# Kernel optimization log

Measured on AMD Instinct MI355X. Metric: run time of the kernel, lower is better.

## Reference

```python
import jax, jax.numpy as jnp
import numpy as np

N_NODES = 50000  # nodes in the (sub)graph


def setup_inputs() -> dict:
    key = jax.random.key(0)
    ks = jax.random.split(key, 8)
    nodes = jax.random.randint(ks[0], (N_NODES,), 0, 100000)
    src = jax.random.randint(ks[1], (800000,), 0, N_NODES)
    dst = jax.random.randint(ks[2], (800000,), 0, N_NODES)
    emb = jax.random.normal(ks[3], (100000, 256), dtype=jnp.float32)
    W = jax.random.normal(ks[4], (256, 128), dtype=jnp.float32) * 0.05
    b = jax.random.normal(ks[5], (128,), dtype=jnp.float32) * 0.05
    mlp_w = jax.random.normal(ks[6], (128, 40), dtype=jnp.float32) * 0.05
    mlp_b = jax.random.normal(ks[7], (40,), dtype=jnp.float32) * 0.05
    return {"nodes": nodes, "src": src, "dst": dst, "emb": emb,
            "W": W, "b": b, "mlp_w": mlp_w, "mlp_b": mlp_b}


def reference(nodes, src, dst, emb, W, b, mlp_w, mlp_b):
    n = N_NODES
    ones = jnp.ones_like(src, dtype=jnp.float32)
    out_deg = jax.ops.segment_sum(ones, src, num_segments=n)  # src out-degree
    in_deg = jax.ops.segment_sum(ones, dst, num_segments=n)   # dst in-degree
    norm_src = jax.lax.rsqrt(jnp.maximum(out_deg, 1.0))       # D_out^{-1/2}
    norm_dst = jax.lax.rsqrt(jnp.maximum(in_deg, 1.0))        # D_in^{-1/2}

    feat = emb[nodes]                                          # [N, in_dim]
    # dgl GraphConv(norm='both'): in_dim > out_dim -> project first, then aggregate
    h = (feat * norm_src[:, None]) @ W                         # [N, out_dim]
    agg = jax.ops.segment_sum(h[src], dst, num_segments=n)     # SpMM: sum over in-edges
    feat_out = agg * norm_dst[:, None] + b                     # [N, out_dim]

    logits = feat_out @ mlp_w + mlp_b                          # [N, num_classes]
    return (feat_out, logits)
```

## Files before the change

### kernel.cpp

```cpp
#include <hip/hip_runtime.h>

#define IN_DIM 256
#define OUT_DIM 128
#define N_CLS 40

#define SLICE 16384
#define NE_CH 40

typedef __attribute__((ext_vector_type(8))) short short8;
typedef __attribute__((ext_vector_type(4))) float floatx4;

static __device__ __forceinline__ unsigned short f2bf(float f) {
    union { float f; unsigned u; } v; v.f = f;
    unsigned r = v.u + 0x7FFF + ((v.u >> 16) & 1);
    return (unsigned short)(r >> 16);
}

static __device__ __forceinline__ unsigned cvtpk(float lo, float hi) {
    unsigned r;
    asm("v_cvt_pk_bf16_f32 %0, %1, %2" : "=v"(r) : "v"(lo), "v"(hi));
    return r;
}

__global__ __launch_bounds__(256) void hist_wconv_kernel(
    const int* __restrict__ src, const int* __restrict__ dst,
    int* __restrict__ partial_out, int* __restrict__ partial_in,
    const float* __restrict__ W, unsigned short* __restrict__ Wt,
    int* __restrict__ done, int ne, int n, int chunk, int nbh)
{
    __shared__ __align__(16) int lh_out[SLICE];
    __shared__ __align__(16) int lh_in[SLICE];

    const int tid = threadIdx.x;

    if (blockIdx.x >= nbh) {
        if (blockIdx.x == (unsigned)nbh && tid == 0) *done = 0;
        int t = (blockIdx.x - nbh) * 256 + tid;
        if (t < IN_DIM * OUT_DIM) {
            int k = t >> 7, c = t & 127;
            Wt[c * IN_DIM + k] = f2bf(W[t]);
        }
        return;
    }

    const int s = blockIdx.x / NE_CH;
    const int e = blockIdx.x % NE_CH;
    const int lo = s * SLICE;
    const int hi = min(lo + SLICE, n);

    for (int i = tid; i < SLICE; i += 256) { lh_out[i] = 0; lh_in[i] = 0; }
    __syncthreads();

    const int start = e * chunk;
    const int end = min(start + chunk, ne);
    const int cnt4 = (end - start) >> 2;
    const int4* s4 = (const int4*)(src + start);
    const int4* d4 = (const int4*)(dst + start);
    for (int k = tid; k < cnt4; k += 256) {
        int4 sv = s4[k];
        int4 dv = d4[k];
        unsigned q;
        q = (unsigned)(sv.x - lo); if (q < SLICE) atomicAdd(&lh_out[q], 1);
        q = (unsigned)(sv.y - lo); if (q < SLICE) atomicAdd(&lh_out[q], 1);
        q = (unsigned)(sv.z - lo); if (q < SLICE) atomicAdd(&lh_out[q], 1);
        q = (unsigned)(sv.w - lo); if (q < SLICE) atomicAdd(&lh_out[q], 1);
        q = (unsigned)(dv.x - lo); if (q < SLICE) atomicAdd(&lh_in[q], 1);
        q = (unsigned)(dv.y - lo); if (q < SLICE) atomicAdd(&lh_in[q], 1);
        q = (unsigned)(dv.z - lo); if (q < SLICE) atomicAdd(&lh_in[q], 1);
        q = (unsigned)(dv.w - lo); if (q < SLICE) atomicAdd(&lh_in[q], 1);
    }
    for (int t = start + (cnt4 << 2) + tid; t < end; t += 256) {
        unsigned q;
        q = (unsigned)(src[t] - lo); if (q < SLICE) atomicAdd(&lh_out[q], 1);
        q = (unsigned)(dst[t] - lo); if (q < SLICE) atomicAdd(&lh_in[q], 1);
    }
    __syncthreads();

    const int cnt = hi - lo;
    const int c4 = cnt >> 2;
    int4* po = (int4*)(partial_out + (size_t)e * n + lo);
    int4* pi = (int4*)(partial_in + (size_t)e * n + lo);
    for (int i = tid; i < c4; i += 256) {
        po[i] = ((const int4*)lh_out)[i];
        pi[i] = ((const int4*)lh_in)[i];
    }
    for (int i = (c4 << 2) + tid; i < cnt; i += 256) {
        partial_out[(size_t)e * n + lo + i] = lh_out[i];
        partial_in[(size_t)e * n + lo + i] = lh_in[i];
    }
}

__global__ __launch_bounds__(256) void reduce_scan_kernel(
    int* __restrict__ partial_out, int* __restrict__ partial_in,
    int* __restrict__ cnt_out, int* __restrict__ row_start,
    int* __restrict__ bsum, int* __restrict__ boffs,
    int* __restrict__ done, int n)
{
    __shared__ int wsum[4];
    __shared__ int is_last;
    const int tid = threadIdx.x;
    const int lane = tid & 63, wid = tid >> 6;
    const int base = blockIdx.x * 1024 + tid * 4;

    int4 run = make_int4(0, 0, 0, 0);

    if (base + 4 <= n) {
        int4 sum = make_int4(0, 0, 0, 0);
#pragma unroll
        for (int e = 0; e < NE_CH; e++) {
            int4 v = *(const int4*)(partial_out + (size_t)e * n + base);
            sum.x += v.x; sum.y += v.y; sum.z += v.z; sum.w += v.w;
        }
        *(int4*)(cnt_out + base) = sum;

#pragma unroll
        for (int e = 0; e < NE_CH; e++) {
            int* p = partial_in + (size_t)e * n + base;
            int4 v = *(const int4*)p;
            *(int4*)p = run;
            run.x += v.x; run.y += v.y; run.z += v.z; run.w += v.w;
        }
    } else if (base <= n) {
        int rr[4] = {0, 0, 0, 0};
#pragma unroll
        for (int j = 0; j < 4; j++) {
            int pos = base + j;
            if (pos < n) {
                int sum = 0, r = 0;
                for (int e = 0; e < NE_CH; e++) {
                    sum += partial_out[(size_t)e * n + pos];
                    int v = partial_in[(size_t)e * n + pos];
                    partial_in[(size_t)e * n + pos] = r;
                    r += v;
                }
                cnt_out[pos] = sum;
                rr[j] = r;
            }
        }
        run.x = rr[0]; run.y = rr[1]; run.z = rr[2]; run.w = rr[3];
    }

    const int s = run.x + run.y + run.z + run.w;
    const int e1 = run.x, e2 = run.x + run.y, e3 = run.x + run.y + run.z;

    int incl = s;
#pragma unroll
    for (int off = 1; off < 64; off <<= 1) {
        int q = __shfl_up(incl, (unsigned)off, 64);
        if (lane >= off) incl += q;
    }
    if (lane == 63) wsum[wid] = incl;
    __syncthreads();
    int woff = 0;
    for (int w = 0; w < wid; ++w) woff += wsum[w];
    const int texcl = woff + incl - s;

    if (base + 4 <= n) {
        int4 o = make_int4(texcl, texcl + e1, texcl + e2, texcl + e3);
        *(int4*)(row_start + base) = o;
    } else if (base <= n) {
        const int eo[4] = {0, e1, e2, e3};
#pragma unroll
        for (int j = 0; j < 4; j++) {
            int pos = base + j;
            if (pos <= n) row_start[pos] = texcl + eo[j];
        }
    }
    if (tid == 0) bsum[blockIdx.x] = wsum[0] + wsum[1] + wsum[2] + wsum[3];

    __threadfence();
    if (tid == 0) {
        int prev = atomicAdd(done, 1);
        is_last = (prev == (int)gridDim.x - 1) ? 1 : 0;
    }
    __syncthreads();
    if (is_last && tid < 64) {
        __threadfence();
        const int nb = (int)gridDim.x;
        int carry = 0;
        for (int c = 0; c < nb; c += 64) {
            int i = c + lane;
            int v = (i < nb) ? bsum[i] : 0;
            int inc2 = v;
#pragma unroll
            for (int off = 1; off < 64; off <<= 1) {
                int q = __shfl_up(inc2, (unsigned)off, 64);
                if (lane >= off) inc2 += q;
            }
            if (i < nb) boffs[i] = carry + inc2 - v;
            carry += __shfl(inc2, 63, 64);
        }
        if (lane == 0) boffs[nb] = carry;
    }
}

__global__ __launch_bounds__(256) void scatter_gemm_kernel(
    const int* __restrict__ src, const int* __restrict__ dst,
    const int* __restrict__ row_start, const int* __restrict__ boffs,
    const int* __restrict__ prefix_in, int* __restrict__ csr_src,
    const int* __restrict__ nodes, const float* __restrict__ emb,
    const unsigned short* __restrict__ Wt, const int* __restrict__ cnt_out,
    unsigned short* __restrict__ h,
    int ne, int n, int chunk, int nbh)
{
    __shared__ __align__(16) char smem[SLICE * 4];

    const int tid = threadIdx.x;

    if (blockIdx.x < (unsigned)nbh) {
        int* cur = (int*)smem;
        const int s = blockIdx.x / NE_CH;
        const int e = blockIdx.x % NE_CH;
        const int lo = s * SLICE;
        const int hi = min(lo + SLICE, n);
        const int cnt = hi - lo;

        const int c4 = cnt >> 2;
        for (int i = tid; i < c4; i += 256) {
            int idx4 = lo + i * 4;
            int4 rs = *(const int4*)(row_start + idx4);
            int4 pf = *(const int4*)(prefix_in + (size_t)e * n + idx4);
            const int bo = boffs[idx4 >> 10];
            rs.x += pf.x + bo; rs.y += pf.y + bo;
            rs.z += pf.z + bo; rs.w += pf.w + bo;
            ((int4*)cur)[i] = rs;
        }
        for (int i = (c4 << 2) + tid; i < cnt; i += 256) {
            int pos = lo + i;
            cur[i] = row_start[pos] + boffs[pos >> 10]
                   + prefix_in[(size_t)e * n + pos];
        }
        __syncthreads();

        const int start = e * chunk;
        const int end = min(start + chunk, ne);
        const int cnt4e = (end - start) >> 2;
        const int4* s4 = (const int4*)(src + start);
        const int4* d4 = (const int4*)(dst + start);
        for (int k = tid; k < cnt4e; k += 256) {
            int4 sv = s4[k];
            int4 dv = d4[k];
            unsigned q;
            q = (unsigned)(dv.x - lo); if (q < SLICE) csr_src[atomicAdd(&cur[q], 1)] = sv.x;
            q = (unsigned)(dv.y - lo); if (q < SLICE) csr_src[atomicAdd(&cur[q], 1)] = sv.y;
            q = (unsigned)(dv.z - lo); if (q < SLICE) csr_src[atomicAdd(&cur[q], 1)] = sv.z;
            q = (unsigned)(dv.w - lo); if (q < SLICE) csr_src[atomicAdd(&cur[q], 1)] = sv.w;
        }
        for (int t = start + (cnt4e << 2) + tid; t < end; t += 256) {
            unsigned q = (unsigned)(dst[t] - lo);
            if (q < SLICE) csr_src[atomicAdd(&cur[q], 1)] = src[t];
        }
        return;
    }

    unsigned short* A_lds = (unsigned short*)smem;
    unsigned short* B_lds = (unsigned short*)(smem + 10240);
    int*   snode  = (int*)(smem + 20480);
    float* sscale = (float*)(smem + 20992);

    const int m0 = (blockIdx.x - nbh) * 128;

    if (tid < 128) {
        int gr = m0 + tid;
        snode[tid]  = (gr < n) ? nodes[gr] : 0;
        sscale[tid] = (gr < n) ? rsqrtf(fmaxf((float)cnt_out[gr], 1.0f)) : 0.0f;
    }
    __syncthreads();

    const int arow = tid >> 1, aq = tid & 1;
    const float* aptr = emb + (size_t)snode[arow] * IN_DIM + aq * 16;
    const unsigned short* bptr = Wt + arow * IN_DIM + aq * 16;

    float    ar[16];
    unsigned bw[8];

#define LOAD_REGS(KK) do {                                           \
        _Pragma("unroll")                                            \
        for (int q = 0; q < 4; q++) {                                \
            const floatx4 v = *(const floatx4*)(aptr + (KK) * 32 + q * 4); \
            ar[q*4+0]=v[0]; ar[q*4+1]=v[1]; ar[q*4+2]=v[2]; ar[q*4+3]=v[3]; \
        }                                                            \
        const uint4 w0 = *(const uint4*)(bptr + (KK) * 32);          \
        const uint4 w1 = *(const uint4*)(bptr + (KK) * 32 + 8);      \
        bw[0]=w0.x; bw[1]=w0.y; bw[2]=w0.z; bw[3]=w0.w;              \
        bw[4]=w1.x; bw[5]=w1.y; bw[6]=w1.z; bw[7]=w1.w;              \
    } while (0)

#define WRITE_LDS() do {                                             \
        uint4 uv0, uv1;                                              \
        uv0.x = cvtpk(ar[0],  ar[1]);  uv0.y = cvtpk(ar[2],  ar[3]); \
        uv0.z = cvtpk(ar[4],  ar[5]);  uv0.w = cvtpk(ar[6],  ar[7]); \
        uv1.x = cvtpk(ar[8],  ar[9]);  uv1.y = cvtpk(ar[10], ar[11]);\
        uv1.z = cvtpk(ar[12], ar[13]); uv1.w = cvtpk(ar[14], ar[15]);\
        *(uint4*)&A_lds[arow * 40 + aq * 16]     = uv0;              \
        *(uint4*)&A_lds[arow * 40 + aq * 16 + 8] = uv1;              \
        uint4 b0, b1;                                                \
        b0.x=bw[0]; b0.y=bw[1]; b0.z=bw[2]; b0.w=bw[3];              \
        b1.x=bw[4]; b1.y=bw[5]; b1.z=bw[6]; b1.w=bw[7];              \
        *(uint4*)&B_lds[arow * 40 + aq * 16]     = b0;               \
        *(uint4*)&B_lds[arow * 40 + aq * 16 + 8] = b1;               \
    } while (0)

    const int wave = tid >> 6, lane = tid & 63;
    const int wr = (wave & 1) * 64;
    const int wc = (wave >> 1) * 64;
    const int fr = lane & 15;
    const int koff = (lane >> 4) * 8;

    floatx4 acc[4][4];
#pragma unroll
    for (int i = 0; i < 4; i++)
#pragma unroll
        for (int j = 0; j < 4; j++) acc[i][j] = (floatx4){0.f, 0.f, 0.f, 0.f};

    LOAD_REGS(0);
    WRITE_LDS();

    for (int kk = 0; kk < 8; ++kk) {
        if (kk < 7) LOAD_REGS(kk + 1);
        __syncthreads();
        short8 af[4], bf[4];
#pragma unroll
        for (int t = 0; t < 4; t++) {
            af[t] = *(const short8*)&A_lds[(wr + t * 16 + fr) * 40 + koff];
            bf[t] = *(const short8*)&B_lds[(wc + t * 16 + fr) * 40 + koff];
        }
#pragma unroll
        for (int rt = 0; rt < 4; rt++)
#pragma unroll
            for (int ct = 0; ct < 4; ct++)
                acc[rt][ct] = __builtin_amdgcn_mfma_f32_16x16x32_bf16(
                    bf[ct], af[rt], acc[rt][ct], 0, 0, 0);
        __syncthreads();
        if (kk < 7) WRITE_LDS();
    }

#pragma unroll
    for (int rt = 0; rt < 4; rt++) {
        int lrow = wr + rt * 16 + fr;
        int grow = m0 + lrow;
        float sc = sscale[lrow];
        if (grow < n) {
#pragma unroll
            for (int ct = 0; ct < 4; ct++) {
                int col = wc + ct * 16 + (lane >> 4) * 4;
                uint2 o;
                o.x = cvtpk(acc[rt][ct][0] * sc, acc[rt][ct][1] * sc);
                o.y = cvtpk(acc[rt][ct][2] * sc, acc[rt][ct][3] * sc);
                *(uint2*)&h[(size_t)grow * OUT_DIM + col] = o;
            }
        }
    }
#undef LOAD_REGS
#undef WRITE_LDS
}

__global__ __launch_bounds__(256) void spmm_csr_kernel(
    const int* __restrict__ row_start, const int* __restrict__ boffs,
    const int* __restrict__ csr_src, const unsigned short* __restrict__ h,
    const float* __restrict__ bias, float* __restrict__ out_feat, int n)
{
    const int lane = threadIdx.x & 63;
    const int c2 = lane * 2;
    const int row = blockIdx.x * 4 + (threadIdx.x >> 6);
    if (row >= n) return;

    const int rs = row_start[row]     + boffs[row >> 10];
    const int re = row_start[row + 1] + boffs[(row + 1) >> 10];
    const int deg = re - rs;

    float aL[4] = {0.f, 0.f, 0.f, 0.f};
    float aH[4] = {0.f, 0.f, 0.f, 0.f};

    for (int base = 0; base < deg; base += 64) {
        const int cnt = min(deg - base, 64);
        int idx = (lane < cnt) ? csr_src[rs + base + lane] : 0;
        int t = 0;
        for (; t + 15 < cnt; t += 16) {
            int s[16];
#pragma unroll
            for (int u = 0; u < 16; u++) s[u] = __shfl(idx, t + u, 64);
            unsigned v[16];
#pragma unroll
            for (int u = 0; u < 16; u++)
                v[u] = *(const unsigned*)&h[(size_t)s[u] * OUT_DIM + c2];
#pragma unroll
            for (int u = 0; u < 16; u++) {
                union { unsigned uu; float f; } x, y;
                x.uu = v[u] << 16;
                y.uu = v[u] & 0xffff0000u;
                aL[u & 3] += x.f;
                aH[u & 3] += y.f;
            }
        }
        for (; t + 3 < cnt; t += 4) {
            int s[4];
#pragma unroll
            for (int u = 0; u < 4; u++) s[u] = __shfl(idx, t + u, 64);
            unsigned v[4];
#pragma unroll
            for (int u = 0; u < 4; u++)
                v[u] = *(const unsigned*)&h[(size_t)s[u] * OUT_DIM + c2];
#pragma unroll
            for (int u = 0; u < 4; u++) {
                union { unsigned uu; float f; } x, y;
                x.uu = v[u] << 16;
                y.uu = v[u] & 0xffff0000u;
                aL[u] += x.f;
                aH[u] += y.f;
            }
        }
        for (; t < cnt; ++t) {
            int s0 = __shfl(idx, t, 64);
            unsigned v0 = *(const unsigned*)&h[(size_t)s0 * OUT_DIM + c2];
            union { unsigned uu; float f; } x, y;
            x.uu = v0 << 16;
            y.uu = v0 & 0xffff0000u;
            aL[0] += x.f;
            aH[0] += y.f;
        }
    }

    const float nd = rsqrtf(fmaxf((float)deg, 1.0f));
    const float f0 = ((aL[0] + aL[1]) + (aL[2] + aL[3])) * nd + bias[c2];
    const float f1 = ((aH[0] + aH[1]) + (aH[2] + aH[3])) * nd + bias[c2 + 1];
    union { float f[2]; unsigned long long u; } o;
    o.f[0] = f0; o.f[1] = f1;
    __builtin_nontemporal_store(o.u,
        (unsigned long long*)&out_feat[(size_t)row * OUT_DIM + c2]);
}

__global__ __launch_bounds__(256) void mlp_mfma_kernel(
    const float* __restrict__ F, const float* __restrict__ mlp_w,
    const float* __restrict__ mlp_b, float* __restrict__ out_logits, int n)
{
    __shared__ unsigned short A_lds[48 * 136];
    __shared__ float s_mlpb[48];

    const int tid = threadIdx.x;
    for (int i = tid; i < 48 * 128; i += 256) {
        int cls = i >> 7, k = i & 127;
        A_lds[cls * 136 + k] =
            (cls < N_CLS) ? f2bf(mlp_w[(size_t)k * N_CLS + cls]) : (unsigned short)0;
    }
    if (tid < 48) s_mlpb[tid] = (tid < N_CLS) ? mlp_b[tid] : 0.f;
    __syncthreads();

    const int wave = tid >> 6, lane = tid & 63;
    const int r = lane & 15, koff = (lane >> 4) * 8;
    const int row = blockIdx.x * 64 + wave * 16 + r;
    const int rowc = (row < n) ? row : (n - 1);
    const float* fp = F + (size_t)rowc * OUT_DIM + koff;

    floatx4 acc[3];
#pragma unroll
    for (int ct = 0; ct < 3; ct++) acc[ct] = (floatx4){0.f, 0.f, 0.f, 0.f};

#pragma unroll
    for (int kk = 0; kk < 4; kk++) {
        floatx4 v0 = *(const floatx4*)(fp + kk * 32);
        floatx4 v1 = *(const floatx4*)(fp + kk * 32 + 4);
        union { unsigned u32[4]; short8 v; } bfr;
        bfr.u32[0] = cvtpk(v0[0], v0[1]);
        bfr.u32[1] = cvtpk(v0[2], v0[3]);
        bfr.u32[2] = cvtpk(v1[0], v1[1]);
        bfr.u32[3] = cvtpk(v1[2], v1[3]);
#pragma unroll
        for (int ct = 0; ct < 3; ct++) {
            short8 af = *(const short8*)&A_lds[(ct * 16 + r) * 136 + kk * 32 + koff];
            acc[ct] = __builtin_amdgcn_mfma_f32_16x16x32_bf16(af, bfr.v, acc[ct], 0, 0, 0);
        }
    }

    if (row < n) {
#pragma unroll
        for (int ct = 0; ct < 3; ct++)
#pragma unroll
            for (int i = 0; i < 4; i++) {
                int cls = ct * 16 + (lane >> 4) * 4 + i;
                if (cls < N_CLS)
                    __builtin_nontemporal_store(acc[ct][i] + s_mlpb[cls],
                        &out_logits[(size_t)row * N_CLS + cls]);
            }
    }
}

extern "C" void kernel_launch(void* const* d_in, const int* in_sizes, int n_in,
                              void* d_out, int out_size, void* d_ws, size_t ws_size,
                              hipStream_t stream) {
    const int*   nodes = (const int*)d_in[0];
    const int*   src   = (const int*)d_in[1];
    const int*   dst   = (const int*)d_in[2];
    const float* emb   = (const float*)d_in[3];
    const float* W     = (const float*)d_in[4];
    const float* b     = (const float*)d_in[5];
    const float* mlp_w = (const float*)d_in[6];
    const float* mlp_b = (const float*)d_in[7];

    const int n  = in_sizes[0];
    const int ne = in_sizes[1];

    int* cnt_out     = (int*)d_ws;
    int* bsum        = cnt_out + n;
    int* boffs       = bsum + 512;
    int* done        = boffs + 512;
    int* row_start   = done + 8;
    int* csr_src     = row_start + n + 8;
    int* partial_out = csr_src + ne;
    int* partial_in  = partial_out + (size_t)NE_CH * n;
    size_t off = ((size_t)(2 * n + 1048) + (size_t)ne + 2 * (size_t)NE_CH * n) * sizeof(int);
    off = (off + 15) & ~(size_t)15;
    unsigned short* Wt = (unsigned short*)((char*)d_ws + off);
    off += (size_t)IN_DIM * OUT_DIM * sizeof(unsigned short);
    off = (off + 15) & ~(size_t)15;
    unsigned short* h = (unsigned short*)((char*)d_ws + off);

    float* out_feat   = (float*)d_out;
    float* out_logits = out_feat + (size_t)n * OUT_DIM;

    const int ns = (n + SLICE - 1) / SLICE;
    const int chunk = (((ne + NE_CH - 1) / NE_CH) + 3) & ~3;
    const int nbh = ns * NE_CH;
    const int nbw = (IN_DIM * OUT_DIM + 255) / 256;
    const int nb = (n + 1023) / 1024;
    const int ngb = (n + 127) / 128;

    hist_wconv_kernel<<<nbh + nbw, 256, 0, stream>>>(
        src, dst, partial_out, partial_in, W, Wt, done, ne, n, chunk, nbh);
    reduce_scan_kernel<<<nb, 256, 0, stream>>>(
        partial_out, partial_in, cnt_out, row_start, bsum, boffs, done, n);
    scatter_gemm_kernel<<<nbh + ngb, 256, 0, stream>>>(
        src, dst, row_start, boffs, partial_in, csr_src,
        nodes, emb, Wt, cnt_out, h, ne, n, chunk, nbh);
    spmm_csr_kernel<<<(n + 3) / 4, 256, 0, stream>>>(
        row_start, boffs, csr_src, h, b, out_feat, n);
    mlp_mfma_kernel<<<(n + 63) / 64, 256, 0, stream>>>(
        out_feat, mlp_w, mlp_b, out_logits, n);
}
```

Before: 126.4 us.

## Fuse SpMM aggregation with MLP logits kernel and enlarge histogram slice

Merges the CSR SpMM kernel and the MLP MFMA kernel into one 512-thread kernel. Each block aggregates 32 rows, keeps them as bf16 in LDS, then runs the 40-class projection with MFMA straight from LDS. This removes a launch and the re-read of out_feat from global memory. The histogram SLICE also grows so 50000 nodes fit in fewer slices, which cuts block count but raises LDS use per block. The costs are that every block re-converts mlp_w, and the barrier makes all rows wait for the slowest row's gather.

After: 137.2 us. 1.09x slower.

```diff
diff --git a/kernel.cpp b/kernel.cpp
--- a/kernel.cpp
+++ b/kernel.cpp
@@ -4,7 +4,7 @@
 #define OUT_DIM 128
 #define N_CLS 40
 
-#define SLICE 16384
+#define SLICE 20352
 #define NE_CH 40
 
 typedef __attribute__((ext_vector_type(8))) short short8;
@@ -33,7 +33,7 @@
 
     const int tid = threadIdx.x;
 
-    if (blockIdx.x >= nbh) {
+    if (blockIdx.x >= (unsigned)nbh) {
         if (blockIdx.x == (unsigned)nbh && tid == 0) *done = 0;
         int t = (blockIdx.x - nbh) * 256 + tid;
         if (t < IN_DIM * OUT_DIM) {
@@ -355,133 +355,128 @@
 #undef WRITE_LDS
 }
 
-__global__ __launch_bounds__(256) void spmm_csr_kernel(
+__global__ __launch_bounds__(512) void spmm_mlp_kernel(
     const int* __restrict__ row_start, const int* __restrict__ boffs,
     const int* __restrict__ csr_src, const unsigned short* __restrict__ h,
-    const float* __restrict__ bias, float* __restrict__ out_feat, int n)
+    const float* __restrict__ bias, const float* __restrict__ mlp_w,
+    const float* __restrict__ mlp_b,
+    float* __restrict__ out_feat, float* __restrict__ out_logits, int n)
 {
-    const int lane = threadIdx.x & 63;
+    __shared__ unsigned short s_fo[32][136];
+    __shared__ unsigned short s_w[48 * 136];
+    __shared__ float s_mlpb[48];
+
+    const int tid = threadIdx.x;
+    const int wave = tid >> 6, lane = tid & 63;
+    const int m0 = blockIdx.x * 32;
+
+    for (int i = tid; i < 48 * 128; i += 512) {
+        int cls = i >> 7, k = i & 127;
+        s_w[cls * 136 + k] =
+            (cls < N_CLS) ? f2bf(mlp_w[(size_t)k * N_CLS + cls]) : (unsigned short)0;
+    }
+    if (tid < 48) s_mlpb[tid] = (tid < N_CLS) ? mlp_b[tid] : 0.f;
+
     const int c2 = lane * 2;
-    const int row = blockIdx.x * 4 + (threadIdx.x >> 6);
-    if (row >= n) return;
-
-    const int rs = row_start[row]     + boffs[row >> 10];
-    const int re = row_start[row + 1] + boffs[(row + 1) >> 10];
-    const int deg = re - rs;
-
-    float aL[4] = {0.f, 0.f, 0.f, 0.f};
-    float aH[4] = {0.f, 0.f, 0.f, 0.f};
-
-    for (int base = 0; base < deg; base += 64) {
-        const int cnt = min(deg - base, 64);
-        int idx = (lane < cnt) ? csr_src[rs + base + lane] : 0;
-        int t = 0;
-        for (; t + 15 < cnt; t += 16) {
-            int s[16];
-#pragma unroll
-            for (int u = 0; u < 16; u++) s[u] = __shfl(idx, t + u, 64);
-            unsigned v[16];
-#pragma unroll
-            for (int u = 0; u < 16; u++)
-                v[u] = *(const unsigned*)&h[(size_t)s[u] * OUT_DIM + c2];
-#pragma unroll
-            for (int u = 0; u < 16; u++) {
-                union { unsigned uu; float f; } x, y;
-                x.uu = v[u] << 16;
-                y.uu = v[u] & 0xffff0000u;
-                aL[u & 3] += x.f;
-                aH[u & 3] += y.f;
+    const float bi0 = bias[c2], bi1 = bias[c2 + 1];
+
+#pragma unroll
+    for (int r = 0; r < 4; r++) {
+        const int lr = wave * 4 + r;
+        const int row = m0 + lr;
+        if (row < n) {
+            const int rs = row_start[row]     + boffs[row >> 10];
+            const int re = row_start[row + 1] + boffs[(row + 1) >> 10];
+            const int deg = re - rs;
+
+            float aL[4] = {0.f, 0.f, 0.f, 0.f};
+            float aH[4] = {0.f, 0.f, 0.f, 0.f};
+
+            for (int base = 0; base < deg; base += 64) {
+                const int cnt = min(deg - base, 64);
+                int idx = (lane < cnt) ? csr_src[rs + base + lane] : 0;
+                int t = 0;
+                for (; t + 15 < cnt; t += 16) {
+                    int s[16];
+#pragma unroll
+                    for (int u = 0; u < 16; u++) s[u] = __shfl(idx, t + u, 64);
+                    unsigned v[16];
+#pragma unroll
+                    for (int u = 0; u < 16; u++)
+                        v[u] = *(const unsigned*)&h[(size_t)s[u] * OUT_DIM + c2];
+#pragma unroll
+                    for (int u = 0; u < 16; u++) {
+                        union { unsigned uu; float f; } x, y;
+                        x.uu = v[u] << 16;
+                        y.uu = v[u] & 0xffff0000u;
+                        aL[u & 3] += x.f;
+                        aH[u & 3] += y.f;
+                    }
+                }
+                for (; t + 3 < cnt; t += 4) {
+                    int s[4];
+#pragma unroll
+                    for (int u = 0; u < 4; u++) s[u] = __shfl(idx, t + u, 64);
+                    unsigned v[4];
+#pragma unroll
+                    for (int u = 0; u < 4; u++)
+                        v[u] = *(const unsigned*)&h[(size_t)s[u] * OUT_DIM + c2];
+#pragma unroll
+                    for (int u = 0; u < 4; u++) {
+                        union { unsigned uu; float f; } x, y;
+                        x.uu = v[u] << 16;
+                        y.uu = v[u] & 0xffff0000u;
+                        aL[u] += x.f;
+                        aH[u] += y.f;
+                    }
+                }
+                for (; t < cnt; ++t) {
+                    int s0 = __shfl(idx, t, 64);
+                    unsigned v0 = *(const unsigned*)&h[(size_t)s0 * OUT_DIM + c2];
+                    union { unsigned uu; float f; } x, y;
+                    x.uu = v0 << 16;
+                    y.uu = v0 & 0xffff0000u;
+                    aL[0] += x.f;
+                    aH[0] += y.f;
+                }
             }
-        }
-        for (; t + 3 < cnt; t += 4) {
-            int s[4];
-#pragma unroll
-            for (int u = 0; u < 4; u++) s[u] = __shfl(idx, t + u, 64);
-            unsigned v[4];
-#pragma unroll
-            for (int u = 0; u < 4; u++)
-                v[u] = *(const unsigned*)&h[(size_t)s[u] * OUT_DIM + c2];
-#pragma unroll
-            for (int u = 0; u < 4; u++) {
-                union { unsigned uu; float f; } x, y;
-                x.uu = v[u] << 16;
-                y.uu = v[u] & 0xffff0000u;
-                aL[u] += x.f;
-                aH[u] += y.f;
-            }
-        }
-        for (; t < cnt; ++t) {
-            int s0 = __shfl(idx, t, 64);
-            unsigned v0 = *(const unsigned*)&h[(size_t)s0 * OUT_DIM + c2];
-            union { unsigned uu; float f; } x, y;
-            x.uu = v0 << 16;
-            y.uu = v0 & 0xffff0000u;
-            aL[0] += x.f;
-            aH[0] += y.f;
-        }
-    }
-
-    const float nd = rsqrtf(fmaxf((float)deg, 1.0f));
-    const float f0 = ((aL[0] + aL[1]) + (aL[2] + aL[3])) * nd + bias[c2];
-    const float f1 = ((aH[0] + aH[1]) + (aH[2] + aH[3])) * nd + bias[c2 + 1];
-    union { float f[2]; unsigned long long u; } o;
-    o.f[0] = f0; o.f[1] = f1;
-    __builtin_nontemporal_store(o.u,
-        (unsigned long long*)&out_feat[(size_t)row * OUT_DIM + c2]);
-}
-
-__global__ __launch_bounds__(256) void mlp_mfma_kernel(
-    const float* __restrict__ F, const float* __restrict__ mlp_w,
-    const float* __restrict__ mlp_b, float* __restrict__ out_logits, int n)
-{
-    __shared__ unsigned short A_lds[48 * 136];
-    __shared__ float s_mlpb[48];
-
-    const int tid = threadIdx.x;
-    for (int i = tid; i < 48 * 128; i += 256) {
-        int cls = i >> 7, k = i & 127;
-        A_lds[cls * 136 + k] =
-            (cls < N_CLS) ? f2bf(mlp_w[(size_t)k * N_CLS + cls]) : (unsigned short)0;
-    }
-    if (tid < 48) s_mlpb[tid] = (tid < N_CLS) ? mlp_b[tid] : 0.f;
+
+            const float nd = rsqrtf(fmaxf((float)deg, 1.0f));
+            const float f0 = ((aL[0] + aL[1]) + (aL[2] + aL[3])) * nd + bi0;
+            const float f1 = ((aH[0] + aH[1]) + (aH[2] + aH[3])) * nd + bi1;
+            union { float f[2]; unsigned long long u; } o;
+            o.f[0] = f0; o.f[1] = f1;
+            __builtin_nontemporal_store(o.u,
+                (unsigned long long*)&out_feat[(size_t)row * OUT_DIM + c2]);
+            *(unsigned*)&s_fo[lr][c2] = cvtpk(f0, f1);
+        } else {
+            *(unsigned*)&s_fo[lr][c2] = 0u;
+        }
+    }
     __syncthreads();
 
-    const int wave = tid >> 6, lane = tid & 63;
-    const int r = lane & 15, koff = (lane >> 4) * 8;
-    const int row = blockIdx.x * 64 + wave * 16 + r;
-    const int rowc = (row < n) ? row : (n - 1);
-    const float* fp = F + (size_t)rowc * OUT_DIM + koff;
-
-    floatx4 acc[3];
-#pragma unroll
-    for (int ct = 0; ct < 3; ct++) acc[ct] = (floatx4){0.f, 0.f, 0.f, 0.f};
-
-#pragma unroll
-    for (int kk = 0; kk < 4; kk++) {
-        floatx4 v0 = *(const floatx4*)(fp + kk * 32);
-        floatx4 v1 = *(const floatx4*)(fp + kk * 32 + 4);
-        union { unsigned u32[4]; short8 v; } bfr;
-        bfr.u32[0] = cvtpk(v0[0], v0[1]);
-        bfr.u32[1] = cvtpk(v0[2], v0[3]);
-        bfr.u32[2] = cvtpk(v1[0], v1[1]);
-        bfr.u32[3] = cvtpk(v1[2], v1[3]);
-#pragma unroll
-        for (int ct = 0; ct < 3; ct++) {
-            short8 af = *(const short8*)&A_lds[(ct * 16 + r) * 136 + kk * 32 + koff];
-            acc[ct] = __builtin_amdgcn_mfma_f32_16x16x32_bf16(af, bfr.v, acc[ct], 0, 0, 0);
-        }
-    }
-
-    if (row < n) {
-#pragma unroll
-        for (int ct = 0; ct < 3; ct++)
+    if (wave < 6) {
+        const int rg = wave / 3, ct = wave - rg * 3;
+        const int r16 = lane & 15, koff = (lane >> 4) * 8;
+
+        floatx4 acc = (floatx4){0.f, 0.f, 0.f, 0.f};
+#pragma unroll
+        for (int kk = 0; kk < 4; kk++) {
+            short8 af = *(const short8*)&s_w[(ct * 16 + r16) * 136 + kk * 32 + koff];
+            short8 bf = *(const short8*)&s_fo[rg * 16 + r16][kk * 32 + koff];
+            acc = __builtin_amdgcn_mfma_f32_16x16x32_bf16(af, bf, acc, 0, 0, 0);
+        }
+
+        const int row = m0 + rg * 16 + r16;
+        if (row < n) {
 #pragma unroll
             for (int i = 0; i < 4; i++) {
                 int cls = ct * 16 + (lane >> 4) * 4 + i;
                 if (cls < N_CLS)
-                    __builtin_nontemporal_store(acc[ct][i] + s_mlpb[cls],
+                    __builtin_nontemporal_store(acc[i] + s_mlpb[cls],
                         &out_logits[(size_t)row * N_CLS + cls]);
             }
+        }
     }
 }
 
@@ -532,8 +527,7 @@
     scatter_gemm_kernel<<<nbh + ngb, 256, 0, stream>>>(
         src, dst, row_start, boffs, partial_in, csr_src,
         nodes, emb, Wt, cnt_out, h, ne, n, chunk, nbh);
-    spmm_csr_kernel<<<(n + 3) / 4, 256, 0, stream>>>(
-        row_start, boffs, csr_src, h, b, out_feat, n);
-    mlp_mfma_kernel<<<(n + 63) / 64, 256, 0, stream>>>(
-        out_feat, mlp_w, mlp_b, out_logits, n);
-}
+    spmm_mlp_kernel<<<(n + 31) / 32, 512, 0, stream>>>(
+        row_start, boffs, csr_src, h, b, mlp_w, mlp_b,
+        out_feat, out_logits, n);
+}
```
